# Kernel optimization log

Measured on AMD Instinct MI355X. Metric: run time of the kernel, lower is better.

## Reference

```python
import jax, jax.numpy as jnp
import numpy as np

N_HEADS = 16
D_EMB = 1024
D_HEAD = D_EMB // N_HEADS


def setup_inputs() -> dict:
    key = jax.random.key(0)
    ks = jax.random.split(key, 5)
    scale = 1.0 / np.sqrt(D_EMB)
    x = jax.random.normal(ks[0], (4, 2048, D_EMB), dtype=jnp.float32)
    W_in = jax.random.normal(ks[1], (3 * D_EMB, D_EMB), dtype=jnp.float32) * scale
    b_in = jax.random.normal(ks[2], (3 * D_EMB,), dtype=jnp.float32) * 0.01
    W_out = jax.random.normal(ks[3], (D_EMB, D_EMB), dtype=jnp.float32) * scale
    b_out = jax.random.normal(ks[4], (D_EMB,), dtype=jnp.float32) * 0.01
    return {"x": x, "W_in": W_in, "b_in": b_in, "W_out": W_out, "b_out": b_out}


def reference(x, W_in, b_in, W_out, b_out):
    b, s, d = x.shape
    qkv = x @ W_in.T + b_in  # [b, s, 3d]
    q, k, v = jnp.split(qkv, 3, axis=-1)
    def heads(t):
        return t.reshape(b, s, N_HEADS, D_HEAD).transpose(0, 2, 1, 3)  # [b,h,s,dh]
    q, k, v = heads(q), heads(k), heads(v)
    scores = jnp.einsum('bhqd,bhkd->bhqk', q, k)
    causal = jnp.tril(jnp.ones((s, s), dtype=bool))  # keep lower-triangular incl diag
    scores = jnp.where(causal, scores, -jnp.inf)
    scores = scores / np.sqrt(D_HEAD).astype(np.float32)
    w = jax.nn.softmax(scores, axis=-1)
    out = jnp.einsum('bhqk,bhkd->bhqd', w, v)  # [b,h,s,dh]
    out = out.transpose(0, 2, 1, 3).reshape(b, s, d)
    return out @ W_out.T + b_out
```

## Files before the change

### kernel.cpp

```cpp
#include <hip/hip_runtime.h>
#include <hip/hip_bf16.h>
#include <cstdint>


typedef float  floatx4  __attribute__((ext_vector_type(4)));
typedef __bf16 bf16x8   __attribute__((ext_vector_type(8)));
typedef __bf16 bf16x4   __attribute__((ext_vector_type(4)));
typedef unsigned short ushortx8 __attribute__((ext_vector_type(8)));

#define MFMA16(a,b,c) __builtin_amdgcn_mfma_f32_16x16x32_bf16(a, b, c, 0, 0, 0)

#define C_SCALE 0.18033688011112042f
#define M_STATIC 16.0f

__device__ __forceinline__ void gload_lds16(const void* g, void* l) {
  __builtin_amdgcn_global_load_lds(
      (__attribute__((address_space(1))) void*)(g),
      (__attribute__((address_space(3))) void*)(l), 16, 0, 0);
}

__global__ __launch_bounds__(256) void cast_kernel(
    const float* __restrict__ in, __bf16* __restrict__ out, int n4) {
  int i = blockIdx.x * 256 + threadIdx.x;
  if (i < n4) {
    const float4 v = ((const float4*)in)[i];
    bf16x4 o;
    o.x = (__bf16)v.x; o.y = (__bf16)v.y; o.z = (__bf16)v.z; o.w = (__bf16)v.w;
    ((bf16x4*)out)[i] = o;
  }
}

__global__ __launch_bounds__(256) void cast_win(
    const float* __restrict__ in, __bf16* __restrict__ out, int n4) {
  int i = blockIdx.x * 256 + threadIdx.x;
  if (i < n4) {
    const float4 v = ((const float4*)in)[i];
    const float s = (i < (1024 * 1024 / 4)) ? C_SCALE : 1.0f;
    bf16x4 o;
    o.x = (__bf16)(v.x * s); o.y = (__bf16)(v.y * s);
    o.z = (__bf16)(v.z * s); o.w = (__bf16)(v.w * s);
    ((bf16x4*)out)[i] = o;
  }
}

__global__ __launch_bounds__(256) void scale_bin(
    const float* __restrict__ in, float* __restrict__ out) {
  int i = blockIdx.x * 256 + threadIdx.x;
  out[i] = in[i] * (i < 1024 ? C_SCALE : 1.0f);
}

template <int MODE>
__global__ __launch_bounds__(256) void gemm_bt(
    const __bf16* __restrict__ A, const __bf16* __restrict__ B,
    const float* __restrict__ bias, void* __restrict__ Cout,
    __bf16* __restrict__ Vt, int M, int N, int K) {
  __shared__ __bf16 As[128 * 32];
  __shared__ __bf16 Bs[128 * 32];
  const int tid = threadIdx.x;
  const int wave = tid >> 6, lane = tid & 63;
  const int quad = lane >> 4, l15 = lane & 15;
  const int wm = (wave & 1) * 64, wn = (wave >> 1) * 64;
  const long row0 = (long)blockIdx.y * 128;
  const long col0 = (long)blockIdx.x * 128;

  floatx4 acc[4][4] = {};

  const int sr = wave * 16 + (lane >> 2);
  const int sc = (lane & 3) * 8;
  const __bf16* ga = A + (row0 + sr) * (long)K + sc;
  const __bf16* gb = B + (col0 + sr) * (long)K + sc;
  __bf16* lA = As + wave * 512 + lane * 8;
  __bf16* lB = Bs + wave * 512 + lane * 8;

  for (int k0 = 0; k0 < K; k0 += 32) {
    gload_lds16(ga,                lA);
    gload_lds16(ga + 64 * (long)K, lA + 2048);
    gload_lds16(gb,                lB);
    gload_lds16(gb + 64 * (long)K, lB + 2048);
    ga += 32; gb += 32;
    __syncthreads();

    bf16x8 af[4], bfr[4];
#pragma unroll
    for (int i = 0; i < 4; ++i)
      af[i] = *(const bf16x8*)(As + (wm + i * 16 + l15) * 32 + quad * 8);
#pragma unroll
    for (int j = 0; j < 4; ++j)
      bfr[j] = *(const bf16x8*)(Bs + (wn + j * 16 + l15) * 32 + quad * 8);
#pragma unroll
    for (int i = 0; i < 4; ++i)
#pragma unroll
      for (int j = 0; j < 4; ++j)
        acc[i][j] = MFMA16(af[i], bfr[j], acc[i][j]);
    __syncthreads();
  }

#pragma unroll
  for (int i = 0; i < 4; ++i) {
    const long r0 = row0 + wm + i * 16 + quad * 4;
#pragma unroll
    for (int j = 0; j < 4; ++j) {
      const long c = col0 + wn + j * 16 + l15;
      const float bv = bias[c];
      if (MODE == 0) {
#pragma unroll
        for (int reg = 0; reg < 4; ++reg)
          ((float*)Cout)[(r0 + reg) * (long)N + c] = acc[i][j][reg] + bv;
      } else {
        if (c < 2048) {
#pragma unroll
          for (int reg = 0; reg < 4; ++reg)
            ((__bf16*)Cout)[(r0 + reg) * (long)N + c] =
                (__bf16)(acc[i][j][reg] + bv);
        } else {
          const int cc = (int)c - 2048;
          const int hh = cc >> 6, dh = cc & 63;
          const int bb = (int)(r0 >> 11), s = (int)(r0 & 2047);
          bf16x4 pk;
#pragma unroll
          for (int reg = 0; reg < 4; ++reg)
            pk[reg] = (__bf16)(acc[i][j][reg] + bv);
          *(bf16x4*)(Vt + ((long)(bb * 16 + hh) * 64 + dh) * 2048 + s) = pk;
        }
      }
    }
  }
}

__global__ __launch_bounds__(512, 4) void flash_attn(
    const __bf16* __restrict__ qkv,
    const __bf16* __restrict__ Vt,
    __bf16* __restrict__ Out) {
  constexpr int S = 2048;
  const int x = blockIdx.x;
  const int h = blockIdx.y, b = blockIdx.z;
  const int qtA = x, qtB = 15 - x;
  const int kmaxA = 2 * qtA + 2;
  const int kmax  = 2 * qtB + 2;

  __shared__ __bf16 Ks[2][64 * 72];
  __shared__ __bf16 Vs[2][64 * 72];
  __shared__ __bf16 Ps[8 * 16 * 72];

  const int tid = threadIdx.x, wave = tid >> 6, lane = tid & 63;
  const int quad = lane >> 4, l15 = lane & 15;

  bf16x8 qf[2][2];
  {
    const long qrA = (long)(b * S + qtA * 128 + wave * 16 + l15) * 3072 + h * 64;
    const long qrB = (long)(b * S + qtB * 128 + wave * 16 + l15) * 3072 + h * 64;
    qf[0][0] = *(const bf16x8*)(qkv + qrA + quad * 8);
    qf[0][1] = *(const bf16x8*)(qkv + qrA + 32 + quad * 8);
    qf[1][0] = *(const bf16x8*)(qkv + qrB + quad * 8);
    qf[1][1] = *(const bf16x8*)(qkv + qrB + 32 + quad * 8);
  }

  bf16x8 ones;
#pragma unroll
  for (int j = 0; j < 8; ++j) ones[j] = (__bf16)1.0f;

  floatx4 oA[4] = {}, oB[4] = {};
  floatx4 lA = {0.f, 0.f, 0.f, 0.f}, lB = {0.f, 0.f, 0.f, 0.f};

  const int srow = tid >> 3;
  const int sc8 = (tid & 7) * 8;
  const __bf16* ka = qkv + ((long)(b * S) + srow) * 3072 + 1024 + h * 64 + sc8;
  const __bf16* va = Vt + ((long)(b * 16 + h) * 64 + srow) * S + sc8;
  const int sl = srow * 72 + sc8;

  __bf16* pw = Ps + wave * 16 * 72;

  ushortx8 kr = *(const ushortx8*)ka;
  ushortx8 vr = *(const ushortx8*)va;
  *(ushortx8*)(&Ks[0][sl]) = kr;
  *(ushortx8*)(&Vs[0][sl]) = vr;
  kr = *(const ushortx8*)(ka + (long)64 * 3072);
  vr = *(const ushortx8*)(va + 64);
  __syncthreads();

  for (int kt = 0; kt < kmax; ++kt) {
    const int cur = kt & 1;
    if (kt + 1 < kmax) {
      *(ushortx8*)(&Ks[cur ^ 1][sl]) = kr;
      *(ushortx8*)(&Vs[cur ^ 1][sl]) = vr;
    }
    if (kt + 2 < kmax) {
      kr = *(const ushortx8*)(ka + (long)(kt + 2) * 64 * 3072);
      vr = *(const ushortx8*)(va + (kt + 2) * 64);
    }

    const bool actA = (kt < kmaxA) && !(kt == 2 * qtA + 1 && wave < 4);
    const bool actB = !(kt == 2 * qtB + 1 && wave < 4);
    const bool partA = actA &&
        ((kt == 2 * qtA && wave < 4) || (kt == 2 * qtA + 1 && wave >= 4));
    const bool partB = actB &&
        ((kt == 2 * qtB && wave < 4) || (kt == 2 * qtB + 1 && wave >= 4));

    floatx4 svA[4], svB[4];
#pragma unroll
    for (int nb = 0; nb < 4; ++nb) {
      const bf16x8 k0 = *(const bf16x8*)(&Ks[cur][(nb * 16 + l15) * 72 + quad * 8]);
      const bf16x8 k1 = *(const bf16x8*)(&Ks[cur][(nb * 16 + l15) * 72 + 32 + quad * 8]);
      if (actA) {
        floatx4 z = {0.f, 0.f, 0.f, 0.f};
        z = MFMA16(qf[0][0], k0, z);
        z = MFMA16(qf[0][1], k1, z);
        svA[nb] = z;
      }
      if (actB) {
        floatx4 z = {0.f, 0.f, 0.f, 0.f};
        z = MFMA16(qf[1][0], k0, z);
        z = MFMA16(qf[1][1], k1, z);
        svB[nb] = z;
      }
    }

    if (partA) {
      const int q0 = qtA * 128 + wave * 16 + quad * 4;
#pragma unroll
      for (int nb = 0; nb < 4; ++nb) {
        const int keyg = kt * 64 + nb * 16 + l15;
#pragma unroll
        for (int r = 0; r < 4; ++r)
          if (keyg > q0 + r) svA[nb][r] = -1.0e30f;
      }
    }
    if (partB) {
      const int q0 = qtB * 128 + wave * 16 + quad * 4;
#pragma unroll
      for (int nb = 0; nb < 4; ++nb) {
        const int keyg = kt * 64 + nb * 16 + l15;
#pragma unroll
        for (int r = 0; r < 4; ++r)
          if (keyg > q0 + r) svB[nb][r] = -1.0e30f;
      }
    }

    bf16x8 paA0, paA1, paB0, paB1;
    if (actA) {
#pragma unroll
      for (int nb = 0; nb < 4; ++nb)
#pragma unroll
        for (int r = 0; r < 4; ++r)
          pw[(quad * 4 + r) * 72 + nb * 16 + l15] =
              (__bf16)exp2f(svA[nb][r] - M_STATIC);
      paA0 = *(const bf16x8*)(pw + l15 * 72 + quad * 8);
      paA1 = *(const bf16x8*)(pw + l15 * 72 + 32 + quad * 8);
      lA = MFMA16(paA0, ones, lA);
      lA = MFMA16(paA1, ones, lA);
    }
    if (actB) {
#pragma unroll
      for (int nb = 0; nb < 4; ++nb)
#pragma unroll
        for (int r = 0; r < 4; ++r)
          pw[(quad * 4 + r) * 72 + nb * 16 + l15] =
              (__bf16)exp2f(svB[nb][r] - M_STATIC);
      paB0 = *(const bf16x8*)(pw + l15 * 72 + quad * 8);
      paB1 = *(const bf16x8*)(pw + l15 * 72 + 32 + quad * 8);
      lB = MFMA16(paB0, ones, lB);
      lB = MFMA16(paB1, ones, lB);
    }

#pragma unroll
    for (int nb = 0; nb < 4; ++nb) {
      const bf16x8 v0 = *(const bf16x8*)(&Vs[cur][(nb * 16 + l15) * 72 + quad * 8]);
      const bf16x8 v1 = *(const bf16x8*)(&Vs[cur][(nb * 16 + l15) * 72 + 32 + quad * 8]);
      if (actA) {
        oA[nb] = MFMA16(paA0, v0, oA[nb]);
        oA[nb] = MFMA16(paA1, v1, oA[nb]);
      }
      if (actB) {
        oB[nb] = MFMA16(paB0, v0, oB[nb]);
        oB[nb] = MFMA16(paB1, v1, oB[nb]);
      }
    }
    __syncthreads();
  }

  {
    const long orow0 = (long)(b * S + qtA * 128 + wave * 16 + quad * 4);
#pragma unroll
    for (int r = 0; r < 4; ++r) {
      const float inv = 1.f / lA[r];
#pragma unroll
      for (int nb = 0; nb < 4; ++nb)
        Out[(orow0 + r) * 1024 + h * 64 + nb * 16 + l15] =
            (__bf16)(oA[nb][r] * inv);
    }
  }
  {
    const long orow0 = (long)(b * S + qtB * 128 + wave * 16 + quad * 4);
#pragma unroll
    for (int r = 0; r < 4; ++r) {
      const float inv = 1.f / lB[r];
#pragma unroll
      for (int nb = 0; nb < 4; ++nb)
        Out[(orow0 + r) * 1024 + h * 64 + nb * 16 + l15] =
            (__bf16)(oB[nb][r] * inv);
    }
  }
}

extern "C" void kernel_launch(void* const* d_in, const int* in_sizes, int n_in,
                              void* d_out, int out_size, void* d_ws, size_t ws_size,
                              hipStream_t stream) {
  const float* x     = (const float*)d_in[0];
  const float* W_in  = (const float*)d_in[1];
  const float* b_in  = (const float*)d_in[2];
  const float* W_out = (const float*)d_in[3];
  const float* b_out = (const float*)d_in[4];

  const int BS = 4 * 2048;
  const int D = 1024, N3 = 3072;

  char* w = (char*)d_ws;
  __bf16* xb    = (__bf16*)w;  w += (size_t)BS * D * 2;
  __bf16* Winb  = (__bf16*)w;  w += (size_t)N3 * D * 2;
  __bf16* Woutb = (__bf16*)w;  w += (size_t)D * D * 2;
  __bf16* qkvb  = (__bf16*)w;  w += (size_t)BS * N3 * 2;
  __bf16* Vtb   = (__bf16*)w;  w += (size_t)64 * 64 * 2048 * 2;
  __bf16* attnb = (__bf16*)w;  w += (size_t)BS * D * 2;
  float*  bins  = (float*)w;   w += (size_t)N3 * 4;

  cast_kernel<<<dim3((BS * D / 4 + 255) / 256), 256, 0, stream>>>(x, xb, BS * D / 4);
  cast_win   <<<dim3((N3 * D / 4 + 255) / 256), 256, 0, stream>>>(W_in, Winb, N3 * D / 4);
  cast_kernel<<<dim3((D * D / 4 + 255) / 256), 256, 0, stream>>>(W_out, Woutb, D * D / 4);
  scale_bin  <<<dim3(N3 / 256), 256, 0, stream>>>(b_in, bins);

  gemm_bt<2><<<dim3(N3 / 128, BS / 128), 256, 0, stream>>>(
      xb, Winb, bins, (void*)qkvb, Vtb, BS, N3, D);

  flash_attn<<<dim3(8, 16, 4), 512, 0, stream>>>(qkvb, Vtb, attnb);

  gemm_bt<0><<<dim3(D / 128, BS / 128), 256, 0, stream>>>(
      attnb, Woutb, b_out, d_out, nullptr, BS, D, D);
}
```

Baseline: 305.8 us.

## Transpose score MFMA to keep P in registers, drop LDS P round-trip

Swaps the operands of the QK^T MFMA so each lane holds scores for one query row across keys. This lets the exponentiated probabilities be fed straight into 16x16x16 bf16 MFMAs as the B operand for the PV product, with V as the A operand. The per-wave LDS scratch buffer for P and the ones-vector MFMA used for row sums are removed, and row sums are now computed with in-lane adds plus two cross-lane shuffles. In exchange the PV product uses twice as many half-K MFMAs with 8-byte LDS reads of V, and the output is written as packed 4-element bf16 vectors.

```diff
diff --git a/kernel.cpp b/kernel.cpp
--- a/kernel.cpp
+++ b/kernel.cpp
@@ -6,9 +6,32 @@
 typedef float  floatx4  __attribute__((ext_vector_type(4)));
 typedef __bf16 bf16x8   __attribute__((ext_vector_type(8)));
 typedef __bf16 bf16x4   __attribute__((ext_vector_type(4)));
+typedef short  shortx4  __attribute__((ext_vector_type(4)));
+typedef unsigned int   uint32x2 __attribute__((ext_vector_type(2)));
 typedef unsigned short ushortx8 __attribute__((ext_vector_type(8)));
 
 #define MFMA16(a,b,c) __builtin_amdgcn_mfma_f32_16x16x32_bf16(a, b, c, 0, 0, 0)
+
+__device__ __forceinline__ floatx4 mfma_k16(bf16x4 a, bf16x4 b, floatx4 c) {
+#if defined(__HIP_DEVICE_COMPILE__)
+#if __has_builtin(__builtin_amdgcn_mfma_f32_16x16x16_bf16)
+  return __builtin_amdgcn_mfma_f32_16x16x16_bf16(a, b, c, 0, 0, 0);
+#elif __has_builtin(__builtin_amdgcn_mfma_f32_16x16x16bf16_1k)
+  return __builtin_amdgcn_mfma_f32_16x16x16bf16_1k(
+      __builtin_bit_cast(shortx4, a), __builtin_bit_cast(shortx4, b), c, 0, 0, 0);
+#else
+  floatx4 d;
+  asm("v_mfma_f32_16x16x16_bf16 %0, %1, %2, %3"
+      : "=v"(d)
+      : "v"(__builtin_bit_cast(uint32x2, a)),
+        "v"(__builtin_bit_cast(uint32x2, b)), "v"(c));
+  return d;
+#endif
+#else
+  (void)a; (void)b;
+  return c;
+#endif
+}
 
 #define C_SCALE 0.18033688011112042f
 #define M_STATIC 16.0f
@@ -140,7 +163,6 @@
 
   __shared__ __bf16 Ks[2][64 * 72];
   __shared__ __bf16 Vs[2][64 * 72];
-  __shared__ __bf16 Ps[8 * 16 * 72];
 
   const int tid = threadIdx.x, wave = tid >> 6, lane = tid & 63;
   const int quad = lane >> 4, l15 = lane & 15;
@@ -155,20 +177,14 @@
     qf[1][1] = *(const bf16x8*)(qkv + qrB + 32 + quad * 8);
   }
 
-  bf16x8 ones;
-#pragma unroll
-  for (int j = 0; j < 8; ++j) ones[j] = (__bf16)1.0f;
-
   floatx4 oA[4] = {}, oB[4] = {};
-  floatx4 lA = {0.f, 0.f, 0.f, 0.f}, lB = {0.f, 0.f, 0.f, 0.f};
+  float lAcc[2] = {0.f, 0.f};
 
   const int srow = tid >> 3;
   const int sc8 = (tid & 7) * 8;
   const __bf16* ka = qkv + ((long)(b * S) + srow) * 3072 + 1024 + h * 64 + sc8;
   const __bf16* va = Vt + ((long)(b * 16 + h) * 64 + srow) * S + sc8;
   const int sl = srow * 72 + sc8;
-
-  __bf16* pw = Ps + wave * 16 * 72;
 
   ushortx8 kr = *(const ushortx8*)ka;
   ushortx8 vr = *(const ushortx8*)va;
@@ -203,101 +219,101 @@
       const bf16x8 k1 = *(const bf16x8*)(&Ks[cur][(nb * 16 + l15) * 72 + 32 + quad * 8]);
       if (actA) {
         floatx4 z = {0.f, 0.f, 0.f, 0.f};
-        z = MFMA16(qf[0][0], k0, z);
-        z = MFMA16(qf[0][1], k1, z);
+        z = MFMA16(k0, qf[0][0], z);
+        z = MFMA16(k1, qf[0][1], z);
         svA[nb] = z;
       }
       if (actB) {
         floatx4 z = {0.f, 0.f, 0.f, 0.f};
-        z = MFMA16(qf[1][0], k0, z);
-        z = MFMA16(qf[1][1], k1, z);
+        z = MFMA16(k0, qf[1][0], z);
+        z = MFMA16(k1, qf[1][1], z);
         svB[nb] = z;
       }
     }
 
     if (partA) {
-      const int q0 = qtA * 128 + wave * 16 + quad * 4;
+      const int qg = qtA * 128 + wave * 16 + l15;
 #pragma unroll
       for (int nb = 0; nb < 4; ++nb) {
-        const int keyg = kt * 64 + nb * 16 + l15;
+        const int key0 = kt * 64 + nb * 16 + quad * 4;
 #pragma unroll
         for (int r = 0; r < 4; ++r)
-          if (keyg > q0 + r) svA[nb][r] = -1.0e30f;
+          if (key0 + r > qg) svA[nb][r] = -1.0e30f;
       }
     }
     if (partB) {
-      const int q0 = qtB * 128 + wave * 16 + quad * 4;
+      const int qg = qtB * 128 + wave * 16 + l15;
 #pragma unroll
       for (int nb = 0; nb < 4; ++nb) {
-        const int keyg = kt * 64 + nb * 16 + l15;
+        const int key0 = kt * 64 + nb * 16 + quad * 4;
 #pragma unroll
         for (int r = 0; r < 4; ++r)
-          if (keyg > q0 + r) svB[nb][r] = -1.0e30f;
-      }
-    }
-
-    bf16x8 paA0, paA1, paB0, paB1;
+          if (key0 + r > qg) svB[nb][r] = -1.0e30f;
+      }
+    }
+
+    bf16x4 pfA[4], pfB[4];
     if (actA) {
+      float ls = 0.f;
 #pragma unroll
       for (int nb = 0; nb < 4; ++nb)
 #pragma unroll
-        for (int r = 0; r < 4; ++r)
-          pw[(quad * 4 + r) * 72 + nb * 16 + l15] =
-              (__bf16)exp2f(svA[nb][r] - M_STATIC);
-      paA0 = *(const bf16x8*)(pw + l15 * 72 + quad * 8);
-      paA1 = *(const bf16x8*)(pw + l15 * 72 + 32 + quad * 8);
-      lA = MFMA16(paA0, ones, lA);
-      lA = MFMA16(paA1, ones, lA);
+        for (int r = 0; r < 4; ++r) {
+          const float p = exp2f(svA[nb][r] - M_STATIC);
+          ls += p;
+          pfA[nb][r] = (__bf16)p;
+        }
+      ls += __shfl_xor(ls, 16, 64);
+      ls += __shfl_xor(ls, 32, 64);
+      lAcc[0] += ls;
     }
     if (actB) {
+      float ls = 0.f;
 #pragma unroll
       for (int nb = 0; nb < 4; ++nb)
 #pragma unroll
-        for (int r = 0; r < 4; ++r)
-          pw[(quad * 4 + r) * 72 + nb * 16 + l15] =
-              (__bf16)exp2f(svB[nb][r] - M_STATIC);
-      paB0 = *(const bf16x8*)(pw + l15 * 72 + quad * 8);
-      paB1 = *(const bf16x8*)(pw + l15 * 72 + 32 + quad * 8);
-      lB = MFMA16(paB0, ones, lB);
-      lB = MFMA16(paB1, ones, lB);
-    }
-
-#pragma unroll
-    for (int nb = 0; nb < 4; ++nb) {
-      const bf16x8 v0 = *(const bf16x8*)(&Vs[cur][(nb * 16 + l15) * 72 + quad * 8]);
-      const bf16x8 v1 = *(const bf16x8*)(&Vs[cur][(nb * 16 + l15) * 72 + 32 + quad * 8]);
-      if (actA) {
-        oA[nb] = MFMA16(paA0, v0, oA[nb]);
-        oA[nb] = MFMA16(paA1, v1, oA[nb]);
-      }
-      if (actB) {
-        oB[nb] = MFMA16(paB0, v0, oB[nb]);
-        oB[nb] = MFMA16(paB1, v1, oB[nb]);
+        for (int r = 0; r < 4; ++r) {
+          const float p = exp2f(svB[nb][r] - M_STATIC);
+          ls += p;
+          pfB[nb][r] = (__bf16)p;
+        }
+      ls += __shfl_xor(ls, 16, 64);
+      ls += __shfl_xor(ls, 32, 64);
+      lAcc[1] += ls;
+    }
+
+#pragma unroll
+    for (int mb = 0; mb < 4; ++mb) {
+#pragma unroll
+      for (int c = 0; c < 4; ++c) {
+        const bf16x4 vf = *(const bf16x4*)(&Vs[cur][(mb * 16 + l15) * 72 + c * 16 + quad * 4]);
+        if (actA) oA[mb] = mfma_k16(vf, pfA[c], oA[mb]);
+        if (actB) oB[mb] = mfma_k16(vf, pfB[c], oB[mb]);
       }
     }
     __syncthreads();
   }
 
   {
-    const long orow0 = (long)(b * S + qtA * 128 + wave * 16 + quad * 4);
-#pragma unroll
-    for (int r = 0; r < 4; ++r) {
-      const float inv = 1.f / lA[r];
-#pragma unroll
-      for (int nb = 0; nb < 4; ++nb)
-        Out[(orow0 + r) * 1024 + h * 64 + nb * 16 + l15] =
-            (__bf16)(oA[nb][r] * inv);
+    const float inv = 1.f / lAcc[0];
+    const long row = (long)(b * S + qtA * 128 + wave * 16 + l15);
+#pragma unroll
+    for (int mb = 0; mb < 4; ++mb) {
+      bf16x4 pk;
+#pragma unroll
+      for (int r = 0; r < 4; ++r) pk[r] = (__bf16)(oA[mb][r] * inv);
+      *(bf16x4*)(Out + row * 1024 + h * 64 + mb * 16 + quad * 4) = pk;
     }
   }
   {
-    const long orow0 = (long)(b * S + qtB * 128 + wave * 16 + quad * 4);
-#pragma unroll
-    for (int r = 0; r < 4; ++r) {
-      const float inv = 1.f / lB[r];
-#pragma unroll
-      for (int nb = 0; nb < 4; ++nb)
-        Out[(orow0 + r) * 1024 + h * 64 + nb * 16 + l15] =
-            (__bf16)(oB[nb][r] * inv);
+    const float inv = 1.f / lAcc[1];
+    const long row = (long)(b * S + qtB * 128 + wave * 16 + l15);
+#pragma unroll
+    for (int mb = 0; mb < 4; ++mb) {
+      bf16x4 pk;
+#pragma unroll
+      for (int r = 0; r < 4; ++r) pk[r] = (__bf16)(oB[mb][r] * inv);
+      *(bf16x4*)(Out + row * 1024 + h * 64 + mb * 16 + quad * 4) = pk;
     }
   }
 }
```

Result: slower. 320.8 us (+4.9%).
